# Performance work log

Hardware: AMD Instinct MI355X
Metric: run time of the kernel (lower is better)

## Reference

```python
import jax, jax.numpy as jnp
import numpy as np
from jax.scipy.special import digamma, gammaln

NUM_CLASSES = 3
FOCAL_GAMMA = 2.0
LABEL_SMOOTHING = 0.1
EVIDENTIAL_W = 0.1
CONTRASTIVE_W = 0.1
BOUNDARY_W = 0.15
TRIPLET_W = 0.1
QUALITY_W = 0.1
TRIPLET_MARGIN = 1.5


def setup_inputs() -> dict:
    key = jax.random.key(0)
    k1, k2, k3 = jax.random.split(key, 3)
    B, D = 4096, 512
    logits = jax.random.normal(k1, (B, NUM_CLASSES), dtype=jnp.float32)
    targets = jax.random.randint(k2, (B,), 0, 3)
    features = jax.random.normal(k3, (B, D), dtype=jnp.float32)
    alpha = jax.random.uniform(jax.random.fold_in(key, 7), (B, NUM_CLASSES), dtype=jnp.float32)
    focal_alpha = jnp.array([1.0, 2.0, 1.5], dtype=jnp.float32)
    class_weights = jnp.array([1.0, 2.0, 1.5], dtype=jnp.float32)
    return {"logits": logits, "targets": targets, "features": features,
            "alpha": alpha, "epoch": 1, "focal_alpha": focal_alpha,
            "class_weights": class_weights}


def reference(logits, targets, features, alpha, epoch, focal_alpha, class_weights):
    B = logits.shape[0]
    C = NUM_CLASSES

    # ---- focal loss (label-smoothed CE, torch semantics) ----
    logp = jax.nn.log_softmax(logits, axis=1)                      # [B,C]
    nll = -jnp.take_along_axis(logp, targets[:, None], axis=1)[:, 0]
    ce_ls = (1.0 - LABEL_SMOOTHING) * nll + LABEL_SMOOTHING * (-logp.mean(axis=1))
    pt = jnp.exp(-ce_ls)
    focal = (focal_alpha[targets] * (1.0 - pt) ** FOCAL_GAMMA * ce_ls).mean()

    # ---- weighted CE (torch weighted mean: sum(w*nll)/sum(w)) ----
    w = class_weights[targets]
    ce = (w * nll).sum() / w.sum()

    # ---- enhanced boundary loss ----
    probs = jax.nn.softmax(logits, axis=1)
    real = targets == 0
    semi = targets == 1
    syn = targets == 2
    rb = jnp.where(real, probs[:, 1] + 0.6 * probs[:, 2], 0.0).sum()
    sb = jnp.where(syn, probs[:, 1] + 0.4 * probs[:, 0], 0.0).sum()
    mb = jnp.where(semi, 1.0 - probs[:, 1] + 0.3 * (probs[:, 0] + probs[:, 2]), 0.0).sum()
    boundary = (rb + sb + 4.5 * mb) / (B + 1e-8)

    total = 0.4 * focal + 0.3 * ce + BOUNDARY_W * boundary

    # ---- normalized features and pairwise cosine-sim matrix ----
    norms = jnp.linalg.norm(features, axis=1, keepdims=True)
    f = features / jnp.maximum(norms, 1e-12)
    sim = f @ f.T                                                  # [B,B]
    same = targets[:, None] == targets[None, :]
    eye = jnp.eye(B, dtype=bool)

    # ---- enhanced contrastive loss ----
    pos = jnp.where(same, (1.0 - sim) ** 2, 0.0).sum()
    neg = jnp.where(~same, jnp.clip(sim - 0.2, 0.0) ** 2, 0.0).sum()
    semi_pair = semi[:, None] & semi[None, :]
    semi_l = jnp.where(semi_pair, (1.0 - sim) ** 2, 0.0).sum()
    contrastive = (pos + neg + 4.0 * semi_l) / (B * B + 1e-8)

    # ---- enhanced triplet loss (batch-hard, vectorized) ----
    d2 = jnp.clip(2.0 - 2.0 * sim, 0.0)
    dist = jnp.sqrt(jnp.where(eye, 1.0, d2))  # diag masked; safe sqrt
    pos_mask = same & ~eye
    neg_mask = ~same
    hp = jnp.max(jnp.where(pos_mask, dist, -jnp.inf), axis=1)
    hn = jnp.min(jnp.where(neg_mask, dist, jnp.inf), axis=1)
    valid = pos_mask.any(axis=1) & neg_mask.any(axis=1)
    margin = TRIPLET_MARGIN * jnp.where(targets == 1, 2.5, 1.0)
    tl = jax.nn.relu(hp - hn + margin)
    cnt = valid.sum()
    triplet = jnp.where(cnt > 0,
                        jnp.where(valid, tl, 0.0).sum() / jnp.maximum(cnt, 1),
                        0.0)

    # ---- quality-invariant loss (upper-tri same-class pairs) ----
    upper = jnp.triu(jnp.ones((B, B), dtype=bool), k=1)
    qmask = same & upper
    npairs = qmask.sum()
    q = jnp.where(qmask, (1.0 - sim) ** 2, 0.0).sum() / jnp.maximum(npairs, 1)
    frac2 = syn.astype(jnp.float32).mean()
    q = q * jnp.where(syn.sum() > 0, 1.0 + 2.5 * frac2, 1.0)
    quality = jnp.where(npairs > 0, q, 0.0)

    # ---- evidential loss ----
    onehot = jax.nn.one_hot(targets, C, dtype=jnp.float32)
    S = alpha.sum(axis=1, keepdims=True) + 1e-8
    likelihood = (onehot * (digamma(S) - digamma(alpha + 1e-8))).sum(axis=1)
    at = onehot + (1.0 - onehot) * alpha
    ats = at.sum(axis=1) + 1e-8
    kl = (gammaln(ats) - gammaln(at + 1e-8).sum(axis=1)
          + ((at - 1.0) * (digamma(at + 1e-8) - digamma(ats[:, None] + 1e-8))).sum(axis=1))
    annealing = min(1.0, (epoch / 25.0) ** 2)
    evidential = likelihood.mean() + annealing * 0.2 * kl.mean()

    total = (total + CONTRASTIVE_W * contrastive + TRIPLET_W * triplet
             + QUALITY_W * quality + EVIDENTIAL_W * evidential)
    return total
```

## Files before the change

kernel.cpp:

```cpp
#include <hip/hip_runtime.h>
#include <hip/hip_bf16.h>
#include <cstdint>

typedef __attribute__((ext_vector_type(8))) __bf16 bf8;
typedef __attribute__((ext_vector_type(4))) float f32x4;

#if defined(__has_builtin)
#if __has_builtin(__builtin_amdgcn_global_load_lds)
#define USE_GLL 1
#endif
#endif
#ifndef USE_GLL
#define USE_GLL 0
#endif

#if USE_GLL
__device__ __forceinline__ void gll16(const __bf16* g, __bf16* l){
  __builtin_amdgcn_global_load_lds(
      (const __attribute__((address_space(1))) void*)g,
      (__attribute__((address_space(3))) void*)l, 16, 0, 0);
}
#endif

__device__ __forceinline__ unsigned mapf(float x){
  unsigned u = __float_as_uint(x);
  return (u & 0x80000000u) ? ~u : (u | 0x80000000u);
}
__device__ __forceinline__ float unmapf(unsigned u){
  return __uint_as_float((u & 0x80000000u) ? (u & 0x7FFFFFFFu) : ~u);
}

__device__ float digammaf_(float x){
  float r = 0.f;
  while (x < 6.f){ r -= 1.f/x; x += 1.f; }
  float inv = 1.f/x, inv2 = inv*inv;
  r += logf(x) - 0.5f*inv
     - inv2*(0.08333333333f - inv2*(0.008333333333f - inv2*0.003968253968f));
  return r;
}

__global__ __launch_bounds__(256) void k_prep(const float* __restrict__ feat,
    __bf16* __restrict__ fb2,
    const float* __restrict__ logits, const int* __restrict__ targets,
    const float* __restrict__ alpha,  const float* __restrict__ fa,
    const float* __restrict__ cw, int B, int D,
    float* __restrict__ psum, unsigned* rowMinU, unsigned* rowMaxU){
  int bid = blockIdx.x, tid = threadIdx.x;
  int wave = tid >> 6, lane = tid & 63;
  __shared__ float sloc[4][8];

  int row = bid*4 + wave;
  const float* src = feat + (size_t)row*D;
  float ss = 0.f;
  for (int c = lane*4; c < D; c += 64*4){
    float4 v = *(const float4*)(src + c);
    ss += v.x*v.x + v.y*v.y + v.z*v.z + v.w*v.w;
  }
  #pragma unroll
  for (int off=32; off; off>>=1) ss += __shfl_xor(ss, off);
  float inv = 1.f / fmaxf(sqrtf(ss), 1e-12f);

  int p = row >> 6, r = row & 63;
  int rsw = (r >> 1) & 3;
  for (int c = lane*8; c < D; c += 64*8){
    float4 v0 = *(const float4*)(src + c);
    float4 v1 = *(const float4*)(src + c + 4);
    bf8 o;
    o[0]=(__bf16)(v0.x*inv); o[1]=(__bf16)(v0.y*inv);
    o[2]=(__bf16)(v0.z*inv); o[3]=(__bf16)(v0.w*inv);
    o[4]=(__bf16)(v1.x*inv); o[5]=(__bf16)(v1.y*inv);
    o[6]=(__bf16)(v1.z*inv); o[7]=(__bf16)(v1.w*inv);
    int cc = c >> 5;
    int cb = (c >> 3) & 3;
    size_t off = (size_t)(p*16 + cc)*2048 + r*32 + ((cb ^ rsw)*8);
    *(bf8*)(fb2 + off) = o;
  }

  if (tid < 4){ rowMinU[bid*4+tid] = 0xFFFFFFFFu; rowMaxU[bid*4+tid] = 0u; }

  int i = row;
  float l0=logits[3*i], l1=logits[3*i+1], l2=logits[3*i+2];
  int t = targets[i];
  float m = fmaxf(l0, fmaxf(l1,l2));
  float e0=expf(l0-m), e1=expf(l1-m), e2=expf(l2-m);
  float se = e0+e1+e2;
  float lse = m + logf(se);
  float lp0=l0-lse, lp1=l1-lse, lp2=l2-lse;
  float lpt = (t==0)?lp0:((t==1)?lp1:lp2);
  float nll = -lpt;
  float ce_ls = 0.9f*nll + 0.1f*(-(lp0+lp1+lp2)*(1.f/3.f));
  float pt = expf(-ce_ls);
  float om = 1.f - pt;
  float focal_i = fa[t]*om*om*ce_ls;
  float w = cw[t];
  float ce_n = w*nll, ce_d = w;
  float p0=e0/se, p1=e1/se, p2=e2/se;
  float bnd;
  if (t==0)      bnd = p1 + 0.6f*p2;
  else if (t==2) bnd = p1 + 0.4f*p0;
  else           bnd = 4.5f*(1.f - p1 + 0.3f*(p0+p2));
  float a0=alpha[3*i], a1=alpha[3*i+1], a2=alpha[3*i+2];
  float S = a0+a1+a2 + 1e-8f;
  float at_ = (t==0)?a0:((t==1)?a1:a2);
  float lik = digammaf_(S) - digammaf_(at_ + 1e-8f);
  float b0 = (t==0)?1.f:a0, b1 = (t==1)?1.f:a1, b2 = (t==2)?1.f:a2;
  float ats = b0+b1+b2 + 1e-8f;
  float psa = digammaf_(ats + 1e-8f);
  float kl = lgammaf(ats)
     - (lgammaf(b0+1e-8f)+lgammaf(b1+1e-8f)+lgammaf(b2+1e-8f))
     + (b0-1.f)*(digammaf_(b0+1e-8f)-psa)
     + (b1-1.f)*(digammaf_(b1+1e-8f)-psa)
     + (b2-1.f)*(digammaf_(b2+1e-8f)-psa);
  if (lane == 0){
    sloc[wave][0]=focal_i; sloc[wave][1]=ce_n; sloc[wave][2]=ce_d;
    sloc[wave][3]=bnd;     sloc[wave][4]=lik;  sloc[wave][5]=kl;
  }
  __syncthreads();
  if (tid < 6)
    psum[bid*8+tid] = sloc[0][tid]+sloc[1][tid]+sloc[2][tid]+sloc[3][tid];
}

__global__ __launch_bounds__(64) void k_pairs(const __bf16* __restrict__ fb2,
    const int* __restrict__ targets, int B, int D,
    float* __restrict__ pairPart, unsigned* rowMinU, unsigned* rowMaxU){
  __shared__ __bf16 sA[2][2048];
  __shared__ __bf16 sB[2][2048];

  int t = blockIdx.x;
  int bx = (int)((sqrtf(8.f*(float)t + 1.f) - 1.f)*0.5f);
  while ((bx+1)*(bx+2)/2 <= t) bx++;
  while (bx*(bx+1)/2 > t) bx--;
  int by = t - bx*(bx+1)/2;
  bool isDiag = (by == bx);
  int rowBase = by*64, colBase = bx*64;

  int lane = threadIdx.x;
  int quad = lane >> 4, l16 = lane & 15;
  int NCH = D/32;

  const __bf16* srcA = fb2 + (size_t)by*NCH*2048 + lane*8;
  const __bf16* srcB = fb2 + (size_t)bx*NCH*2048 + lane*8;
  const __bf16* sB0  = isDiag ? &sA[0][0] : &sB[0][0];

  int offA[4];
  #pragma unroll
  for (int mi=0; mi<4; mi++){
    int R = mi*16 + l16;
    offA[mi] = R*32 + ((quad ^ ((R>>1)&3))*8);
  }

  f32x4 C[4][4] = {};

#if USE_GLL
  #define STAGE(buf, it) do{ \
    const __bf16* ga_ = srcA + (it)*2048; \
    gll16(ga_ + 0*512, &sA[buf][0*512]); \
    gll16(ga_ + 1*512, &sA[buf][1*512]); \
    gll16(ga_ + 2*512, &sA[buf][2*512]); \
    gll16(ga_ + 3*512, &sA[buf][3*512]); \
    if (!isDiag){ \
      const __bf16* gb_ = srcB + (it)*2048; \
      gll16(gb_ + 0*512, &sB[buf][0*512]); \
      gll16(gb_ + 1*512, &sB[buf][1*512]); \
      gll16(gb_ + 2*512, &sB[buf][2*512]); \
      gll16(gb_ + 3*512, &sB[buf][3*512]); \
    } \
  }while(0)
#else
  #define STAGE(buf, it) do{ \
    const __bf16* ga_ = srcA + (it)*2048; \
    _Pragma("unroll") \
    for (int j=0; j<4; j++) \
      *(bf8*)&sA[buf][j*512 + lane*8] = *(const bf8*)(ga_ + j*512); \
    if (!isDiag){ \
      const __bf16* gb_ = srcB + (it)*2048; \
      _Pragma("unroll") \
      for (int j=0; j<4; j++) \
        *(bf8*)&sB[buf][j*512 + lane*8] = *(const bf8*)(gb_ + j*512); \
    } \
  }while(0)
#endif

  #define COMPUTE(buf) do{ \
    bf8 aF[4], bF[4]; \
    _Pragma("unroll") \
    for (int mi=0; mi<4; mi++) aF[mi] = *(const bf8*)(&sA[0][0] + (buf)*2048 + offA[mi]); \
    _Pragma("unroll") \
    for (int ni=0; ni<4; ni++) bF[ni] = *(const bf8*)(sB0 + (buf)*2048 + offA[ni]); \
    _Pragma("unroll") \
    for (int mi=0; mi<4; mi++) \
      _Pragma("unroll") \
      for (int ni=0; ni<4; ni++) \
        C[mi][ni] = __builtin_amdgcn_mfma_f32_16x16x32_bf16(aF[mi], bF[ni], C[mi][ni], 0,0,0); \
  }while(0)

  STAGE(0, 0);
  for (int it=0; it<NCH; it+=2){
    STAGE(1, it+1);
    COMPUTE(0);
    if (it+2 < NCH) STAGE(0, it+2);
    COMPUTE(1);
  }

  int tcol[4];
  #pragma unroll
  for (int ni=0; ni<4; ni++) tcol[ni] = targets[colBase + ni*16 + l16];

  float pos=0.f, neg=0.f, semi=0.f, diag=0.f;
  float cmin[4], cmax[4];
  #pragma unroll
  for (int ni=0; ni<4; ni++){ cmin[ni]=2.f; cmax[ni]=-2.f; }

  #pragma unroll
  for (int mi=0; mi<4; mi++){
    #pragma unroll
    for (int r=0; r<4; r++){
      int rl = mi*16 + quad*4 + r;
      int row = rowBase + rl;
      int tr = targets[row];
      float vmin = 2.f, vmax = -2.f;
      #pragma unroll
      for (int ni=0; ni<4; ni++){
        int col = colBase + ni*16 + l16;
        float s = C[mi][ni][r];
        if (tr == tcol[ni]){
          float omv = 1.f - s;
          float q = omv*omv;
          pos += q;
          if (tr == 1) semi += q;
          if (row == col) diag += q;
          else {
            vmin = fminf(vmin, s);
            cmin[ni] = fminf(cmin[ni], s);
          }
        } else {
          float c0 = fmaxf(s - 0.2f, 0.f);
          neg += c0*c0;
          vmax = fmaxf(vmax, s);
          cmax[ni] = fmaxf(cmax[ni], s);
        }
      }
      #pragma unroll
      for (int off=1; off<16; off<<=1){
        vmin = fminf(vmin, __shfl_xor(vmin, off));
        vmax = fmaxf(vmax, __shfl_xor(vmax, off));
      }
      if (l16 == 0){
        atomicMin(&rowMinU[row], mapf(vmin));
        atomicMax(&rowMaxU[row], mapf(vmax));
      }
    }
  }

  if (!isDiag){
    #pragma unroll
    for (int ni=0; ni<4; ni++){
      float cn = cmin[ni], cx = cmax[ni];
      cn = fminf(cn, __shfl_xor(cn, 16)); cn = fminf(cn, __shfl_xor(cn, 32));
      cx = fmaxf(cx, __shfl_xor(cx, 16)); cx = fmaxf(cx, __shfl_xor(cx, 32));
      if (quad == 0){
        int col = colBase + ni*16 + l16;
        atomicMin(&rowMinU[col], mapf(cn));
        atomicMax(&rowMaxU[col], mapf(cx));
      }
    }
  }

  #pragma unroll
  for (int off=32; off; off>>=1){
    pos  += __shfl_xor(pos, off);
    neg  += __shfl_xor(neg, off);
    semi += __shfl_xor(semi, off);
    diag += __shfl_xor(diag, off);
  }
  if (lane == 0){
    float fac = isDiag ? 1.f : 2.f;
    pairPart[blockIdx.x*4+0] = pos*fac;
    pairPart[blockIdx.x*4+1] = neg*fac;
    pairPart[blockIdx.x*4+2] = semi*fac;
    pairPart[blockIdx.x*4+3] = diag;
  }
}

__global__ __launch_bounds__(1024) void k_final(const int* __restrict__ targets,
    const int* __restrict__ epoch_p, int B, int nprep, int nblk,
    const float* __restrict__ pairPart, const float* __restrict__ psum,
    const unsigned* rowMinU, const unsigned* rowMaxU, float* out){
  int tid = threadIdx.x, wave = tid>>6, lane = tid&63;
  __shared__ float redf[16][8];
  __shared__ int   redi[16][4];
  __shared__ float tot6[6];
  __shared__ int   cns[3];
  __shared__ float ptot[4];

  {
    int c0=0,c1=0,c2=0;
    for (int i4 = tid; i4 < B/4; i4 += 1024){
      int4 tv = ((const int4*)targets)[i4];
      c0 += (tv.x==0)+(tv.y==0)+(tv.z==0)+(tv.w==0);
      c1 += (tv.x==1)+(tv.y==1)+(tv.z==1)+(tv.w==1);
      c2 += (tv.x==2)+(tv.y==2)+(tv.z==2)+(tv.w==2);
    }
    #pragma unroll
    for (int off=32; off; off>>=1){
      c0+=__shfl_xor(c0,off); c1+=__shfl_xor(c1,off); c2+=__shfl_xor(c2,off);
    }
    if (lane==0){ redi[wave][0]=c0; redi[wave][1]=c1; redi[wave][2]=c2; }
  }
  {
    float v0=0,v1=0,v2=0,v3=0,v4=0,v5=0;
    for (int s = tid; s < nprep; s += 1024){
      float4 a = *(const float4*)(psum + s*8);
      float4 b = *(const float4*)(psum + s*8 + 4);
      v0+=a.x; v1+=a.y; v2+=a.z; v3+=a.w; v4+=b.x; v5+=b.y;
    }
    #pragma unroll
    for (int off=32; off; off>>=1){
      v0+=__shfl_xor(v0,off); v1+=__shfl_xor(v1,off); v2+=__shfl_xor(v2,off);
      v3+=__shfl_xor(v3,off); v4+=__shfl_xor(v4,off); v5+=__shfl_xor(v5,off);
    }
    if (lane==0){
      redf[wave][0]=v0; redf[wave][1]=v1; redf[wave][2]=v2;
      redf[wave][3]=v3; redf[wave][4]=v4; redf[wave][5]=v5;
    }
  }
  __syncthreads();
  if (tid == 0){
    int c0=0,c1=0,c2=0;
    float v[6]={0,0,0,0,0,0};
    for (int w2=0; w2<16; w2++){
      c0+=redi[w2][0]; c1+=redi[w2][1]; c2+=redi[w2][2];
      for (int j=0;j<6;j++) v[j]+=redf[w2][j];
    }
    cns[0]=c0; cns[1]=c1; cns[2]=c2;
    for (int j=0;j<6;j++) tot6[j]=v[j];
  }
  __syncthreads();

  {
    float p=0,n=0,s2=0,d=0;
    for (int s = tid; s < nblk; s += 1024){
      float4 a = *(const float4*)(pairPart + s*4);
      p+=a.x; n+=a.y; s2+=a.z; d+=a.w;
    }
    #pragma unroll
    for (int off=32; off; off>>=1){
      p+=__shfl_xor(p,off); n+=__shfl_xor(n,off);
      s2+=__shfl_xor(s2,off); d+=__shfl_xor(d,off);
    }
    if (lane==0){ redf[wave][0]=p; redf[wave][1]=n; redf[wave][2]=s2; redf[wave][3]=d; }
  }
  __syncthreads();
  if (tid == 0){
    float a=0,b=0,c=0,e=0;
    for (int w2=0; w2<16; w2++){ a+=redf[w2][0]; b+=redf[w2][1]; c+=redf[w2][2]; e+=redf[w2][3]; }
    ptot[0]=a; ptot[1]=b; ptot[2]=c; ptot[3]=e;
  }
  __syncthreads();

  int n0=cns[0], n1=cns[1], n2=cns[2];

  float tsum = 0.f, tcnt = 0.f;
  for (int i = tid; i < B; i += 1024){
    int t = targets[i];
    int nt = (t==0)?n0:((t==1)?n1:n2);
    if (nt - 1 > 0 && B - nt > 0){
      float mn = unmapf(rowMinU[i]);
      float mx = unmapf(rowMaxU[i]);
      float hp = sqrtf(fmaxf(2.f - 2.f*mn, 0.f));
      float hn = sqrtf(fmaxf(2.f - 2.f*mx, 0.f));
      float margin = 1.5f * ((t==1) ? 2.5f : 1.f);
      float tl = fmaxf(hp - hn + margin, 0.f);
      tsum += tl; tcnt += 1.f;
    }
  }
  #pragma unroll
  for (int off=32; off; off>>=1){ tsum += __shfl_xor(tsum, off); tcnt += __shfl_xor(tcnt, off); }
  if (lane==0){ redf[wave][6]=tsum; redf[wave][7]=tcnt; }
  __syncthreads();

  if (tid==0){
    float ts=0, tn=0;
    for (int w2=0; w2<16; w2++){ ts+=redf[w2][6]; tn+=redf[w2][7]; }
    float triplet = (tn > 0.f) ? ts / fmaxf(tn, 1.f) : 0.f;
    float pos=ptot[0], neg=ptot[1], semi=ptot[2], diag=ptot[3];
    float Bf = (float)B;
    float focal = tot6[0] / Bf;
    float ce = tot6[1] / tot6[2];
    float boundary = tot6[3] / (Bf + 1e-8f);
    float contrastive = (pos + neg + 4.f*semi) / (Bf*Bf + 1e-8f);
    long long npl = ((long long)n0*(n0-1) + (long long)n1*(n1-1) + (long long)n2*(n2-1))/2;
    float qsum = (pos - diag) * 0.5f;
    float q = qsum / (float)(npl > 0 ? npl : 1);
    if (n2 > 0) q *= (1.f + 2.5f * ((float)n2 / Bf));
    float quality = (npl > 0) ? q : 0.f;
    int ep = epoch_p[0];
    float er = (float)ep / 25.f;
    float ann = fminf(1.f, er*er);
    float evidential = tot6[4]/Bf + ann*0.2f*tot6[5]/Bf;
    float total = 0.4f*focal + 0.3f*ce + 0.15f*boundary
                + 0.1f*contrastive + 0.1f*triplet + 0.1f*quality + 0.1f*evidential;
    out[0] = total;
  }
}

extern "C" void kernel_launch(void* const* d_in, const int* in_sizes, int n_in,
                              void* d_out, int out_size, void* d_ws, size_t ws_size,
                              hipStream_t stream){
  const float* logits   = (const float*)d_in[0];
  const int*   targets  = (const int*)d_in[1];
  const float* features = (const float*)d_in[2];
  const float* alpha    = (const float*)d_in[3];
  const int*   epoch    = (const int*)d_in[4];
  const float* fa       = (const float*)d_in[5];
  const float* cw       = (const float*)d_in[6];
  int B = in_sizes[1];
  int D = in_sizes[2] / B;
  int nprep = B/4;
  int T  = B / 64;
  int nblk = T*(T+1)/2;

  char* ws = (char*)d_ws;
  float*    psum     = (float*)(ws);
  float*    pairPart = (float*)(ws + 65536);
  unsigned* rowMinU  = (unsigned*)(ws + 131072);
  unsigned* rowMaxU  = (unsigned*)(ws + 131072 + (size_t)B*4);
  __bf16*   fb2      = (__bf16*)(ws + 131072 + (size_t)B*8);

  k_prep <<<nprep, 256, 0, stream>>>(features, fb2, logits, targets, alpha, fa, cw,
                                     B, D, psum, rowMinU, rowMaxU);
  k_pairs<<<nblk, 64, 0, stream>>>(fb2, targets, B, D, pairPart, rowMinU, rowMaxU);
  k_final<<<1, 1024, 0, stream>>>(targets, epoch, B, nprep, nblk, pairPart, psum,
                                  rowMinU, rowMaxU, (float*)d_out);
}
```

Baseline: 120.0 us.

## Load MFMA operands directly from global and fuse final reduction into last block

```diff
diff --git a/kernel.cpp b/kernel.cpp
--- a/kernel.cpp
+++ b/kernel.cpp
@@ -4,23 +4,6 @@
 
 typedef __attribute__((ext_vector_type(8))) __bf16 bf8;
 typedef __attribute__((ext_vector_type(4))) float f32x4;
-
-#if defined(__has_builtin)
-#if __has_builtin(__builtin_amdgcn_global_load_lds)
-#define USE_GLL 1
-#endif
-#endif
-#ifndef USE_GLL
-#define USE_GLL 0
-#endif
-
-#if USE_GLL
-__device__ __forceinline__ void gll16(const __bf16* g, __bf16* l){
-  __builtin_amdgcn_global_load_lds(
-      (const __attribute__((address_space(1))) void*)g,
-      (__attribute__((address_space(3))) void*)l, 16, 0, 0);
-}
-#endif
 
 __device__ __forceinline__ unsigned mapf(float x){
   unsigned u = __float_as_uint(x);
@@ -44,10 +27,13 @@
     const float* __restrict__ logits, const int* __restrict__ targets,
     const float* __restrict__ alpha,  const float* __restrict__ fa,
     const float* __restrict__ cw, int B, int D,
-    float* __restrict__ psum, unsigned* rowMinU, unsigned* rowMaxU){
+    float* __restrict__ psum, unsigned* rowMinU, unsigned* rowMaxU,
+    unsigned* done){
   int bid = blockIdx.x, tid = threadIdx.x;
   int wave = tid >> 6, lane = tid & 63;
   __shared__ float sloc[4][8];
+
+  if (bid == 0 && tid == 0) *done = 0u;
 
   int row = bid*4 + wave;
   const float* src = feat + (size_t)row*D;
@@ -122,10 +108,10 @@
 
 __global__ __launch_bounds__(64) void k_pairs(const __bf16* __restrict__ fb2,
     const int* __restrict__ targets, int B, int D,
-    float* __restrict__ pairPart, unsigned* rowMinU, unsigned* rowMaxU){
-  __shared__ __bf16 sA[2][2048];
-  __shared__ __bf16 sB[2][2048];
-
+    float* __restrict__ pairPart, unsigned* rowMinU, unsigned* rowMaxU,
+    unsigned* done, int nblk, int nprep,
+    const float* __restrict__ psum, const int* __restrict__ epoch_p,
+    float* __restrict__ out){
   int t = blockIdx.x;
   int bx = (int)((sqrtf(8.f*(float)t + 1.f) - 1.f)*0.5f);
   while ((bx+1)*(bx+2)/2 <= t) bx++;
@@ -138,55 +124,28 @@
   int quad = lane >> 4, l16 = lane & 15;
   int NCH = D/32;
 
-  const __bf16* srcA = fb2 + (size_t)by*NCH*2048 + lane*8;
-  const __bf16* srcB = fb2 + (size_t)bx*NCH*2048 + lane*8;
-  const __bf16* sB0  = isDiag ? &sA[0][0] : &sB[0][0];
-
   int offA[4];
   #pragma unroll
   for (int mi=0; mi<4; mi++){
     int R = mi*16 + l16;
     offA[mi] = R*32 + ((quad ^ ((R>>1)&3))*8);
   }
+  const __bf16* pA[4]; const __bf16* pB[4];
+  #pragma unroll
+  for (int mi=0; mi<4; mi++){
+    pA[mi] = fb2 + (size_t)by*NCH*2048 + offA[mi];
+    pB[mi] = fb2 + (size_t)bx*NCH*2048 + offA[mi];
+  }
 
   f32x4 C[4][4] = {};
-
-#if USE_GLL
-  #define STAGE(buf, it) do{ \
-    const __bf16* ga_ = srcA + (it)*2048; \
-    gll16(ga_ + 0*512, &sA[buf][0*512]); \
-    gll16(ga_ + 1*512, &sA[buf][1*512]); \
-    gll16(ga_ + 2*512, &sA[buf][2*512]); \
-    gll16(ga_ + 3*512, &sA[buf][3*512]); \
-    if (!isDiag){ \
-      const __bf16* gb_ = srcB + (it)*2048; \
-      gll16(gb_ + 0*512, &sB[buf][0*512]); \
-      gll16(gb_ + 1*512, &sB[buf][1*512]); \
-      gll16(gb_ + 2*512, &sB[buf][2*512]); \
-      gll16(gb_ + 3*512, &sB[buf][3*512]); \
-    } \
+  bf8 aC[4], bC[4], aN[4], bN[4];
+
+  #define LD(dst, P, it) do{ \
+    _Pragma("unroll") \
+    for (int j=0; j<4; j++) dst[j] = *(const bf8*)(P[j] + (it)*2048); \
   }while(0)
-#else
-  #define STAGE(buf, it) do{ \
-    const __bf16* ga_ = srcA + (it)*2048; \
-    _Pragma("unroll") \
-    for (int j=0; j<4; j++) \
-      *(bf8*)&sA[buf][j*512 + lane*8] = *(const bf8*)(ga_ + j*512); \
-    if (!isDiag){ \
-      const __bf16* gb_ = srcB + (it)*2048; \
-      _Pragma("unroll") \
-      for (int j=0; j<4; j++) \
-        *(bf8*)&sB[buf][j*512 + lane*8] = *(const bf8*)(gb_ + j*512); \
-    } \
-  }while(0)
-#endif
-
-  #define COMPUTE(buf) do{ \
-    bf8 aF[4], bF[4]; \
-    _Pragma("unroll") \
-    for (int mi=0; mi<4; mi++) aF[mi] = *(const bf8*)(&sA[0][0] + (buf)*2048 + offA[mi]); \
-    _Pragma("unroll") \
-    for (int ni=0; ni<4; ni++) bF[ni] = *(const bf8*)(sB0 + (buf)*2048 + offA[ni]); \
+
+  #define COMPUTE(aF, bF) do{ \
     _Pragma("unroll") \
     for (int mi=0; mi<4; mi++) \
       _Pragma("unroll") \
@@ -194,12 +153,12 @@
         C[mi][ni] = __builtin_amdgcn_mfma_f32_16x16x32_bf16(aF[mi], bF[ni], C[mi][ni], 0,0,0); \
   }while(0)
 
-  STAGE(0, 0);
+  LD(aC, pA, 0); LD(bC, pB, 0);
   for (int it=0; it<NCH; it+=2){
-    STAGE(1, it+1);
-    COMPUTE(0);
-    if (it+2 < NCH) STAGE(0, it+2);
-    COMPUTE(1);
+    LD(aN, pA, it+1); LD(bN, pB, it+1);
+    COMPUTE(aC, bC);
+    if (it+2 < NCH){ LD(aC, pA, it+2); LD(bC, pB, it+2); }
+    COMPUTE(aN, bN);
   }
 
   int tcol[4];
@@ -280,124 +239,75 @@
     pairPart[blockIdx.x*4+2] = semi*fac;
     pairPart[blockIdx.x*4+3] = diag;
   }
-}
-
-__global__ __launch_bounds__(1024) void k_final(const int* __restrict__ targets,
-    const int* __restrict__ epoch_p, int B, int nprep, int nblk,
-    const float* __restrict__ pairPart, const float* __restrict__ psum,
-    const unsigned* rowMinU, const unsigned* rowMaxU, float* out){
-  int tid = threadIdx.x, wave = tid>>6, lane = tid&63;
-  __shared__ float redf[16][8];
-  __shared__ int   redi[16][4];
-  __shared__ float tot6[6];
-  __shared__ int   cns[3];
-  __shared__ float ptot[4];
-
-  {
-    int c0=0,c1=0,c2=0;
-    for (int i4 = tid; i4 < B/4; i4 += 1024){
-      int4 tv = ((const int4*)targets)[i4];
-      c0 += (tv.x==0)+(tv.y==0)+(tv.z==0)+(tv.w==0);
-      c1 += (tv.x==1)+(tv.y==1)+(tv.z==1)+(tv.w==1);
-      c2 += (tv.x==2)+(tv.y==2)+(tv.z==2)+(tv.w==2);
-    }
-    #pragma unroll
-    for (int off=32; off; off>>=1){
-      c0+=__shfl_xor(c0,off); c1+=__shfl_xor(c1,off); c2+=__shfl_xor(c2,off);
-    }
-    if (lane==0){ redi[wave][0]=c0; redi[wave][1]=c1; redi[wave][2]=c2; }
-  }
-  {
-    float v0=0,v1=0,v2=0,v3=0,v4=0,v5=0;
-    for (int s = tid; s < nprep; s += 1024){
-      float4 a = *(const float4*)(psum + s*8);
-      float4 b = *(const float4*)(psum + s*8 + 4);
-      v0+=a.x; v1+=a.y; v2+=a.z; v3+=a.w; v4+=b.x; v5+=b.y;
-    }
-    #pragma unroll
-    for (int off=32; off; off>>=1){
-      v0+=__shfl_xor(v0,off); v1+=__shfl_xor(v1,off); v2+=__shfl_xor(v2,off);
-      v3+=__shfl_xor(v3,off); v4+=__shfl_xor(v4,off); v5+=__shfl_xor(v5,off);
-    }
-    if (lane==0){
-      redf[wave][0]=v0; redf[wave][1]=v1; redf[wave][2]=v2;
-      redf[wave][3]=v3; redf[wave][4]=v4; redf[wave][5]=v5;
-    }
-  }
-  __syncthreads();
-  if (tid == 0){
-    int c0=0,c1=0,c2=0;
-    float v[6]={0,0,0,0,0,0};
-    for (int w2=0; w2<16; w2++){
-      c0+=redi[w2][0]; c1+=redi[w2][1]; c2+=redi[w2][2];
-      for (int j=0;j<6;j++) v[j]+=redf[w2][j];
-    }
-    cns[0]=c0; cns[1]=c1; cns[2]=c2;
-    for (int j=0;j<6;j++) tot6[j]=v[j];
-  }
-  __syncthreads();
-
-  {
-    float p=0,n=0,s2=0,d=0;
-    for (int s = tid; s < nblk; s += 1024){
-      float4 a = *(const float4*)(pairPart + s*4);
-      p+=a.x; n+=a.y; s2+=a.z; d+=a.w;
-    }
-    #pragma unroll
-    for (int off=32; off; off>>=1){
-      p+=__shfl_xor(p,off); n+=__shfl_xor(n,off);
-      s2+=__shfl_xor(s2,off); d+=__shfl_xor(d,off);
-    }
-    if (lane==0){ redf[wave][0]=p; redf[wave][1]=n; redf[wave][2]=s2; redf[wave][3]=d; }
-  }
-  __syncthreads();
-  if (tid == 0){
-    float a=0,b=0,c=0,e=0;
-    for (int w2=0; w2<16; w2++){ a+=redf[w2][0]; b+=redf[w2][1]; c+=redf[w2][2]; e+=redf[w2][3]; }
-    ptot[0]=a; ptot[1]=b; ptot[2]=c; ptot[3]=e;
-  }
-  __syncthreads();
-
-  int n0=cns[0], n1=cns[1], n2=cns[2];
-
+
+  __threadfence();
+  unsigned old = 0;
+  if (lane == 0) old = atomicAdd(done, 1u);
+  old = (unsigned)__shfl((int)old, 0);
+  if (old != (unsigned)(nblk - 1)) return;
+  __threadfence();
+
+  int c0=0,c1=0,c2=0;
+  for (int i4 = lane; i4 < B/4; i4 += 64){
+    int4 tv = ((const int4*)targets)[i4];
+    c0 += (tv.x==0)+(tv.y==0)+(tv.z==0)+(tv.w==0);
+    c1 += (tv.x==1)+(tv.y==1)+(tv.z==1)+(tv.w==1);
+    c2 += (tv.x==2)+(tv.y==2)+(tv.z==2)+(tv.w==2);
+  }
+  #pragma unroll
+  for (int off=32; off; off>>=1){
+    c0+=__shfl_xor(c0,off); c1+=__shfl_xor(c1,off); c2+=__shfl_xor(c2,off);
+  }
+  int n0=c0, n1=c1, n2=c2;
+
+  float v0=0,v1=0,v2=0,v3=0,v4=0,v5=0;
+  for (int s = lane; s < nprep; s += 64){
+    float4 a = *(const float4*)(psum + s*8);
+    float4 b = *(const float4*)(psum + s*8 + 4);
+    v0+=a.x; v1+=a.y; v2+=a.z; v3+=a.w; v4+=b.x; v5+=b.y;
+  }
+  float pp=0,nn=0,ss=0,dd=0;
+  for (int s = lane; s < nblk; s += 64){
+    float4 a = *(const float4*)(pairPart + s*4);
+    pp+=a.x; nn+=a.y; ss+=a.z; dd+=a.w;
+  }
   float tsum = 0.f, tcnt = 0.f;
-  for (int i = tid; i < B; i += 1024){
-    int t = targets[i];
-    int nt = (t==0)?n0:((t==1)?n1:n2);
+  for (int i = lane; i < B; i += 64){
+    int tt = targets[i];
+    int nt = (tt==0)?n0:((tt==1)?n1:n2);
     if (nt - 1 > 0 && B - nt > 0){
       float mn = unmapf(rowMinU[i]);
       float mx = unmapf(rowMaxU[i]);
       float hp = sqrtf(fmaxf(2.f - 2.f*mn, 0.f));
       float hn = sqrtf(fmaxf(2.f - 2.f*mx, 0.f));
-      float margin = 1.5f * ((t==1) ? 2.5f : 1.f);
-      float tl = fmaxf(hp - hn + margin, 0.f);
-      tsum += tl; tcnt += 1.f;
+      float margin = 1.5f * ((tt==1) ? 2.5f : 1.f);
+      tsum += fmaxf(hp - hn + margin, 0.f); tcnt += 1.f;
     }
   }
   #pragma unroll
-  for (int off=32; off; off>>=1){ tsum += __shfl_xor(tsum, off); tcnt += __shfl_xor(tcnt, off); }
-  if (lane==0){ redf[wave][6]=tsum; redf[wave][7]=tcnt; }
-  __syncthreads();
-
-  if (tid==0){
-    float ts=0, tn=0;
-    for (int w2=0; w2<16; w2++){ ts+=redf[w2][6]; tn+=redf[w2][7]; }
-    float triplet = (tn > 0.f) ? ts / fmaxf(tn, 1.f) : 0.f;
-    float pos=ptot[0], neg=ptot[1], semi=ptot[2], diag=ptot[3];
+  for (int off=32; off; off>>=1){
+    v0+=__shfl_xor(v0,off); v1+=__shfl_xor(v1,off); v2+=__shfl_xor(v2,off);
+    v3+=__shfl_xor(v3,off); v4+=__shfl_xor(v4,off); v5+=__shfl_xor(v5,off);
+    pp+=__shfl_xor(pp,off); nn+=__shfl_xor(nn,off);
+    ss+=__shfl_xor(ss,off); dd+=__shfl_xor(dd,off);
+    tsum+=__shfl_xor(tsum,off); tcnt+=__shfl_xor(tcnt,off);
+  }
+  if (lane == 0){
+    float triplet = (tcnt > 0.f) ? tsum / fmaxf(tcnt, 1.f) : 0.f;
     float Bf = (float)B;
-    float focal = tot6[0] / Bf;
-    float ce = tot6[1] / tot6[2];
-    float boundary = tot6[3] / (Bf + 1e-8f);
-    float contrastive = (pos + neg + 4.f*semi) / (Bf*Bf + 1e-8f);
+    float focal = v0 / Bf;
+    float ce = v1 / v2;
+    float boundary = v3 / (Bf + 1e-8f);
+    float contrastive = (pp + nn + 4.f*ss) / (Bf*Bf + 1e-8f);
     long long npl = ((long long)n0*(n0-1) + (long long)n1*(n1-1) + (long long)n2*(n2-1))/2;
-    float qsum = (pos - diag) * 0.5f;
+    float qsum = (pp - dd) * 0.5f;
     float q = qsum / (float)(npl > 0 ? npl : 1);
     if (n2 > 0) q *= (1.f + 2.5f * ((float)n2 / Bf));
     float quality = (npl > 0) ? q : 0.f;
     int ep = epoch_p[0];
     float er = (float)ep / 25.f;
     float ann = fminf(1.f, er*er);
-    float evidential = tot6[4]/Bf + ann*0.2f*tot6[5]/Bf;
+    float evidential = v4/Bf + ann*0.2f*v5/Bf;
     float total = 0.4f*focal + 0.3f*ce + 0.15f*boundary
                 + 0.1f*contrastive + 0.1f*triplet + 0.1f*quality + 0.1f*evidential;
     out[0] = total;
@@ -422,14 +332,14 @@
 
   char* ws = (char*)d_ws;
   float*    psum     = (float*)(ws);
+  unsigned* done     = (unsigned*)(ws + 49152);
   float*    pairPart = (float*)(ws + 65536);
   unsigned* rowMinU  = (unsigned*)(ws + 131072);
   unsigned* rowMaxU  = (unsigned*)(ws + 131072 + (size_t)B*4);
   __bf16*   fb2      = (__bf16*)(ws + 131072 + (size_t)B*8);
 
   k_prep <<<nprep, 256, 0, stream>>>(features, fb2, logits, targets, alpha, fa, cw,
-                                     B, D, psum, rowMinU, rowMaxU);
-  k_pairs<<<nblk, 64, 0, stream>>>(fb2, targets, B, D, pairPart, rowMinU, rowMaxU);
-  k_final<<<1, 1024, 0, stream>>>(targets, epoch, B, nprep, nblk, pairPart, psum,
-                                  rowMinU, rowMaxU, (float*)d_out);
-}
+                                     B, D, psum, rowMinU, rowMaxU, done);
+  k_pairs<<<nblk, 64, 0, stream>>>(fb2, targets, B, D, pairPart, rowMinU, rowMaxU,
+                                   done, nblk, nprep, psum, epoch, (float*)d_out);
+}
```

After: 230.1 us. +91.7%, slower.
